# Kernel tuning notes

Hardware: AMD Instinct MI355X
Metric: run time of the kernel (lower is better)

Reference implementation:

```python
import jax, jax.numpy as jnp
import numpy as np

N = 100000      # nodes
E = 1600000     # edges (avg degree 16)
F_IN = 256      # num_features
H2 = 128        # nhid * 2 (layer 1 width)
H = 64          # nhid (layer 2 width)
C = 10          # num_classes


def setup_inputs() -> dict:
    key = jax.random.key(0)
    ks = jax.random.split(key, 8)
    x = jax.random.normal(ks[0], (N, F_IN), dtype=jnp.float32)
    edge_index = jax.random.randint(ks[1], (2, E), 0, N, dtype=jnp.int64)
    W1 = jax.random.normal(ks[2], (F_IN, H2), dtype=jnp.float32) / np.float32(np.sqrt(F_IN))
    b1 = jnp.zeros((H2,), jnp.float32)
    W2 = jax.random.normal(ks[3], (H2, H), dtype=jnp.float32) / np.float32(np.sqrt(H2))
    b2 = jnp.zeros((H,), jnp.float32)
    Wl = jax.random.normal(ks[4], (H, C), dtype=jnp.float32) / np.float32(np.sqrt(H))
    bl = jnp.zeros((C,), jnp.float32)
    return {"x": x, "edge_index": edge_index, "W1": W1, "b1": b1,
            "W2": W2, "b2": b2, "Wl": Wl, "bl": bl}


def reference(x, edge_index, W1, b1, W2, b2, Wl, bl):
    # --- GCN normalization with self-loops (PyG GCNConv default) ---
    loops = jnp.arange(N, dtype=edge_index.dtype)
    src = jnp.concatenate([edge_index[0], loops])  # message sources
    dst = jnp.concatenate([edge_index[1], loops])  # message targets
    deg = jax.ops.segment_sum(jnp.ones(src.shape[0], x.dtype), dst, num_segments=N)
    dinv = jnp.where(deg > 0, jax.lax.rsqrt(deg), 0.0)
    norm = dinv[src] * dinv[dst]                   # [E+N]

    def gcn_conv(h, W, b):
        m = h @ W                                  # transform first (out_channels small)
        agg = jax.ops.segment_sum(m[src] * norm[:, None], dst, num_segments=N)
        return agg + b

    h = jax.nn.relu(gcn_conv(x, W1, b1))           # [N, H2]
    h = jax.nn.relu(gcn_conv(h, W2, b2))           # [N, H]
    logits = h @ Wl + bl                            # [N, C]
    return jax.nn.log_softmax(logits, axis=-1)
```

## Files before the change

kernel.cpp:

```cpp
#include <hip/hip_runtime.h>


typedef unsigned short ushort_t;
typedef unsigned int uint_t;
typedef __attribute__((ext_vector_type(8))) short short8;
typedef __attribute__((ext_vector_type(4))) float floatx4;

static __device__ __forceinline__ ushort_t f2bf(float f) {
    union { float f; uint_t u; } c; c.f = f;
    return (ushort_t)((c.u + 0x8000u) >> 16);
}
static __device__ __forceinline__ float bf2f(ushort_t h) {
    union { uint_t u; float f; } c; c.u = ((uint_t)h) << 16;
    return c.f;
}
static __device__ __forceinline__ float2 up2(uint_t p) {
    union { uint_t u; float f; } lo, hi;
    lo.u = p << 16; hi.u = p & 0xffff0000u;
    return make_float2(lo.f, hi.f);
}
static __device__ __forceinline__ uint_t pk2bf(float a, float b) {
    return ((uint_t)f2bf(b) << 16) | (uint_t)f2bf(a);
}

#define NBMAX 800
#define ECAP  4096

__global__ __launch_bounds__(256) void hist_kernel(
    const int* __restrict__ dst, int* __restrict__ histG, int E, int NB) {
    __shared__ int h[NBMAX];
    for (int i = threadIdx.x; i < NB; i += 256) h[i] = 0;
    __syncthreads();
    int i16 = (blockIdx.x * 256 + threadIdx.x) * 16;
    if (i16 + 15 < E) {
        #pragma unroll
        for (int u = 0; u < 4; u++) {
            int4 d = *(const int4*)(dst + i16 + u * 4);
            atomicAdd(&h[d.x >> 7], 1);
            atomicAdd(&h[d.y >> 7], 1);
            atomicAdd(&h[d.z >> 7], 1);
            atomicAdd(&h[d.w >> 7], 1);
        }
    } else {
        for (int e = i16; e < E; e++) atomicAdd(&h[dst[e] >> 7], 1);
    }
    __syncthreads();
    int* out = histG + (size_t)blockIdx.x * NB;
    for (int i = threadIdx.x; i < NB; i += 256) out[i] = h[i];
}

__global__ __launch_bounds__(256) void scan_bucket(
    int* __restrict__ histG, int* __restrict__ totG, int GB, int NB) {
    int b = blockIdx.x * 256 + threadIdx.x;
    if (b >= NB) return;
    int run = 0;
    int g = 0;
    for (; g + 16 <= GB; g += 16) {
        int vv[16];
        #pragma unroll
        for (int u = 0; u < 16; u++) vv[u] = histG[(size_t)(g + u) * NB + b];
        #pragma unroll
        for (int u = 0; u < 16; u++) {
            histG[(size_t)(g + u) * NB + b] = run;
            run += vv[u];
        }
    }
    for (; g < GB; g++) {
        int v = histG[(size_t)g * NB + b];
        histG[(size_t)g * NB + b] = run;
        run += v;
    }
    totG[b] = run;
}

__global__ void scan_tot(const int* __restrict__ totG, int* __restrict__ bbase,
                         int NB) {
    __shared__ int s[256];
    const int t = threadIdx.x;
    int running = 0;
    int nch = (NB + 255) / 256;
    for (int c = 0; c < nch; c++) {
        int j = c * 256 + t;
        int v = (j < NB) ? totG[j] : 0;
        s[t] = v;
        __syncthreads();
        for (int off = 1; off < 256; off <<= 1) {
            int tmp = (t >= off) ? s[t - off] : 0;
            __syncthreads();
            s[t] += tmp;
            __syncthreads();
        }
        if (j < NB) bbase[j] = s[t] - v + running;
        int ctot = s[255];
        __syncthreads();
        running += ctot;
    }
    if (t == 0) bbase[NB] = running;
}

__global__ __launch_bounds__(256) void scatter_kernel(
    const int* __restrict__ src, const int* __restrict__ dst,
    const int* __restrict__ histG, const int* __restrict__ bbase,
    int* __restrict__ packed, int E, int NB) {
    __shared__ int lbase[NBMAX];
    const int* row = histG + (size_t)blockIdx.x * NB;
    for (int i = threadIdx.x; i < NB; i += 256)
        lbase[i] = bbase[i] + row[i];
    __syncthreads();
    int i16 = (blockIdx.x * 256 + threadIdx.x) * 16;
    if (i16 + 15 < E) {
        #pragma unroll
        for (int u = 0; u < 4; u++) {
            int4 s4 = *(const int4*)(src + i16 + u * 4);
            int4 d4 = *(const int4*)(dst + i16 + u * 4);
            int p;
            p = atomicAdd(&lbase[d4.x >> 7], 1); packed[p] = s4.x | ((d4.x & 127) << 17);
            p = atomicAdd(&lbase[d4.y >> 7], 1); packed[p] = s4.y | ((d4.y & 127) << 17);
            p = atomicAdd(&lbase[d4.z >> 7], 1); packed[p] = s4.z | ((d4.z & 127) << 17);
            p = atomicAdd(&lbase[d4.w >> 7], 1); packed[p] = s4.w | ((d4.w & 127) << 17);
        }
    } else {
        for (int e = i16; e < E; e++) {
            int d = dst[e];
            int p = atomicAdd(&lbase[d >> 7], 1);
            packed[p] = src[e] | ((d & 127) << 17);
        }
    }
}

__global__ __launch_bounds__(256) void bucket_csr(
    const int* __restrict__ packed, const int* __restrict__ bbase,
    int* __restrict__ rowptr, int* __restrict__ csr,
    float* __restrict__ dinv, int N, int NB) {
    __shared__ int ebuf[ECAP];
    __shared__ int cnt[128];
    __shared__ int pl[128];
    __shared__ int s[256];
    const int b = blockIdx.x;
    const int t = threadIdx.x;
    const int lo = bbase[b];
    const int hi = bbase[b + 1];
    int m = hi - lo;
    if (m > ECAP) m = ECAP;
    for (int i = t; i < m; i += 256) ebuf[i] = packed[lo + i];
    if (t < 128) cnt[t] = 0;
    __syncthreads();
    for (int i = t; i < m; i += 256) atomicAdd(&cnt[ebuf[i] >> 17], 1);
    __syncthreads();
    const int node0 = b << 7;
    int c = (t < 128) ? cnt[t] : 0;
    if (t < 128 && node0 + t < N)
        dinv[node0 + t] = rsqrtf((float)(c + 1));
    s[t] = c;
    __syncthreads();
    for (int off = 1; off < 256; off <<= 1) {
        int tmp = (t >= off) ? s[t - off] : 0;
        __syncthreads();
        s[t] += tmp;
        __syncthreads();
    }
    int excl = s[t] - c;
    if (t < 128) {
        pl[t] = excl;
        if (node0 + t <= N) rowptr[node0 + t] = lo + excl;
    }
    __syncthreads();
    for (int i = t; i < m; i += 256) {
        int e = ebuf[i];
        int p = atomicAdd(&pl[e >> 17], 1);
        csr[lo + p] = e & 0x1FFFF;
    }
}

__global__ void wcvt2_kernel(const float* __restrict__ W1, const float* __restrict__ W2,
                             ushort_t* __restrict__ W1t, ushort_t* __restrict__ W2t) {
    int i = blockIdx.x * 256 + threadIdx.x;
    if (i < 256 * 128) {
        int k = i / 128, n = i % 128;
        W1t[n * 256 + k] = f2bf(W1[i]);
    }
    int j = i - 256 * 128;
    if (j >= 0 && j < 128 * 64) {
        int k = j / 64, n = j % 64;
        W2t[n * 128 + k] = f2bf(W2[j]);
    }
}

__global__ __launch_bounds__(256, 4) void gemm1_mfma(
    const float* __restrict__ A, const ushort_t* __restrict__ Bt,
    const float* __restrict__ dinv, ushort_t* __restrict__ out, int M) {
    const int tid = threadIdx.x;
    const int l = tid & 63;
    const int wave = tid >> 6;
    const int lrow = l & 15, hh = l >> 4;
    const int m0 = blockIdx.x * 64 + wave * 16;

    int r0 = m0 + lrow; if (r0 >= M) r0 = M - 1;
    const float* ga = A + (size_t)r0 * 256 + hh * 8;
    const ushort_t* gb = Bt + (size_t)lrow * 256 + hh * 8;

    floatx4 acc[8];
    #pragma unroll
    for (int nt = 0; nt < 8; nt++)
        acc[nt] = (floatx4){0.f, 0.f, 0.f, 0.f};

    #pragma unroll
    for (int kk = 0; kk < 8; kk++) {
        const int k0 = kk * 32;
        float4 u = *(const float4*)(ga + k0);
        float4 v = *(const float4*)(ga + k0 + 4);
        short8 afr;
        afr[0] = (short)f2bf(u.x); afr[1] = (short)f2bf(u.y);
        afr[2] = (short)f2bf(u.z); afr[3] = (short)f2bf(u.w);
        afr[4] = (short)f2bf(v.x); afr[5] = (short)f2bf(v.y);
        afr[6] = (short)f2bf(v.z); afr[7] = (short)f2bf(v.w);
        short8 bfr[8];
        #pragma unroll
        for (int nt = 0; nt < 8; nt++)
            bfr[nt] = *(const short8*)(gb + (size_t)nt * 16 * 256 + k0);
        #pragma unroll
        for (int nt = 0; nt < 8; nt++)
            acc[nt] = __builtin_amdgcn_mfma_f32_16x16x32_bf16(
                afr, bfr[nt], acc[nt], 0, 0, 0);
    }

    const int mbase = m0 + hh * 4;
    float4 dv = *(const float4*)&dinv[mbase];
    float d[4] = {dv.x, dv.y, dv.z, dv.w};
    #pragma unroll
    for (int i = 0; i < 4; i++) {
        int m = mbase + i;
        if (m < M) {
            #pragma unroll
            for (int nt = 0; nt < 8; nt++)
                out[(size_t)m * 128 + nt * 16 + lrow] =
                    f2bf(acc[nt][i] * d[i]);
        }
    }
}

__global__ __launch_bounds__(256, 4) void gemm2_mfma(
    const ushort_t* __restrict__ A, const ushort_t* __restrict__ Bt,
    const float* __restrict__ dinv, ushort_t* __restrict__ out, int M) {
    const int tid = threadIdx.x;
    const int l = tid & 63;
    const int wave = tid >> 6;
    const int lrow = l & 15, hh = l >> 4;
    const int m0 = blockIdx.x * 64 + wave * 16;

    int r0 = m0 + lrow; if (r0 >= M) r0 = M - 1;
    const ushort_t* ga = A + (size_t)r0 * 128 + hh * 8;
    const ushort_t* gb = Bt + (size_t)lrow * 128 + hh * 8;

    floatx4 acc[4];
    #pragma unroll
    for (int nt = 0; nt < 4; nt++)
        acc[nt] = (floatx4){0.f, 0.f, 0.f, 0.f};

    #pragma unroll
    for (int kk = 0; kk < 4; kk++) {
        const int k0 = kk * 32;
        short8 afr = *(const short8*)(ga + k0);
        short8 bfr[4];
        #pragma unroll
        for (int nt = 0; nt < 4; nt++)
            bfr[nt] = *(const short8*)(gb + (size_t)nt * 16 * 128 + k0);
        #pragma unroll
        for (int nt = 0; nt < 4; nt++)
            acc[nt] = __builtin_amdgcn_mfma_f32_16x16x32_bf16(
                afr, bfr[nt], acc[nt], 0, 0, 0);
    }

    const int mbase = m0 + hh * 4;
    float4 dv = *(const float4*)&dinv[mbase];
    float d[4] = {dv.x, dv.y, dv.z, dv.w};
    #pragma unroll
    for (int i = 0; i < 4; i++) {
        int m = mbase + i;
        if (m < M) {
            #pragma unroll
            for (int nt = 0; nt < 4; nt++)
                out[(size_t)m * 64 + nt * 16 + lrow] =
                    f2bf(acc[nt][i] * d[i]);
        }
    }
}

__global__ __launch_bounds__(256) void spmm_relu128(
    const ushort_t* __restrict__ Mm, const int* __restrict__ rowptr,
    const int* __restrict__ csr, const float* __restrict__ dinv,
    const float* __restrict__ bias, ushort_t* __restrict__ out, int n, int doff) {
    int v = (blockIdx.x * 256 + threadIdx.x) >> 6;
    int lane = threadIdx.x & 63;
    if (v >= n) return;
    int jb = rowptr[v];
    int cntn = rowptr[v + 1] - jb;
    const char* Mb = (const char*)Mm;
    const int slot = lane >> 4;
    const int q = lane & 15;
    const uint_t qb = (uint_t)q * 16;

    float2 a0 = {0.f, 0.f}, a1 = a0, a2 = a0, a3 = a0;
    if (slot == 0) {
        uint4 s = *(const uint4*)(Mb + ((size_t)v << 8) + qb);
        a0 = up2(s.x); a1 = up2(s.y); a2 = up2(s.z); a3 = up2(s.w);
    }

    for (int base = 0; base < cntn; base += 64) {
        int m = cntn - base; if (m > 64) m = 64;
        int roff = (base + lane < cntn) ? (csr[jb + base + lane] << 8) : doff;
        int m4 = (m + 3) & ~3;
        int jj = 0;
        for (; jj + 16 <= m4; jj += 16) {
            uint_t o[4];
            #pragma unroll
            for (int t = 0; t < 4; t++)
                o[t] = (uint_t)__shfl(roff, jj + 4 * t + slot) + qb;
            uint4 p[4];
            #pragma unroll
            for (int t = 0; t < 4; t++) p[t] = *(const uint4*)(Mb + o[t]);
            #pragma unroll
            for (int t = 0; t < 4; t++) {
                float2 f;
                f = up2(p[t].x); a0.x += f.x; a0.y += f.y;
                f = up2(p[t].y); a1.x += f.x; a1.y += f.y;
                f = up2(p[t].z); a2.x += f.x; a2.y += f.y;
                f = up2(p[t].w); a3.x += f.x; a3.y += f.y;
            }
        }
        for (; jj < m4; jj += 4) {
            uint_t o = (uint_t)__shfl(roff, jj + slot) + qb;
            uint4 p = *(const uint4*)(Mb + o);
            float2 f;
            f = up2(p.x); a0.x += f.x; a0.y += f.y;
            f = up2(p.y); a1.x += f.x; a1.y += f.y;
            f = up2(p.z); a2.x += f.x; a2.y += f.y;
            f = up2(p.w); a3.x += f.x; a3.y += f.y;
        }
    }
    float r[8] = {a0.x, a0.y, a1.x, a1.y, a2.x, a2.y, a3.x, a3.y};
    #pragma unroll
    for (int i = 0; i < 8; i++) r[i] += __shfl_xor(r[i], 16);
    #pragma unroll
    for (int i = 0; i < 8; i++) r[i] += __shfl_xor(r[i], 32);
    if (slot == 0) {
        float d = dinv[v];
        float4 bv0 = *(const float4*)&bias[q * 8];
        float4 bv1 = *(const float4*)&bias[q * 8 + 4];
        float o0 = fmaxf(d * r[0] + bv0.x, 0.f);
        float o1 = fmaxf(d * r[1] + bv0.y, 0.f);
        float o2 = fmaxf(d * r[2] + bv0.z, 0.f);
        float o3 = fmaxf(d * r[3] + bv0.w, 0.f);
        float o4 = fmaxf(d * r[4] + bv1.x, 0.f);
        float o5 = fmaxf(d * r[5] + bv1.y, 0.f);
        float o6 = fmaxf(d * r[6] + bv1.z, 0.f);
        float o7 = fmaxf(d * r[7] + bv1.w, 0.f);
        uint4 pk;
        pk.x = pk2bf(o0, o1); pk.y = pk2bf(o2, o3);
        pk.z = pk2bf(o4, o5); pk.w = pk2bf(o6, o7);
        *(uint4*)(out + (size_t)v * 128 + q * 8) = pk;
    }
}

__global__ __launch_bounds__(256) void spmm_relu64(
    const ushort_t* __restrict__ Mm, const int* __restrict__ rowptr,
    const int* __restrict__ csr, const float* __restrict__ dinv,
    const float* __restrict__ bias, ushort_t* __restrict__ out, int n, int doff) {
    int v = (blockIdx.x * 256 + threadIdx.x) >> 6;
    int lane = threadIdx.x & 63;
    if (v >= n) return;
    int jb = rowptr[v];
    int cntn = rowptr[v + 1] - jb;
    const char* Mb = (const char*)Mm;
    const int slot = lane >> 3;
    const int q = lane & 7;
    const uint_t qb = (uint_t)q * 16;

    float2 a0 = {0.f, 0.f}, a1 = a0, a2 = a0, a3 = a0;
    if (slot == 0) {
        uint4 s = *(const uint4*)(Mb + ((size_t)v << 7) + qb);
        a0 = up2(s.x); a1 = up2(s.y); a2 = up2(s.z); a3 = up2(s.w);
    }

    for (int base = 0; base < cntn; base += 64) {
        int m = cntn - base; if (m > 64) m = 64;
        int roff = (base + lane < cntn) ? (csr[jb + base + lane] << 7) : doff;
        int m8 = (m + 7) & ~7;
        int jj = 0;
        for (; jj + 16 <= m8; jj += 16) {
            uint_t o[2];
            #pragma unroll
            for (int t = 0; t < 2; t++)
                o[t] = (uint_t)__shfl(roff, jj + 8 * t + slot) + qb;
            uint4 p[2];
            #pragma unroll
            for (int t = 0; t < 2; t++) p[t] = *(const uint4*)(Mb + o[t]);
            #pragma unroll
            for (int t = 0; t < 2; t++) {
                float2 f;
                f = up2(p[t].x); a0.x += f.x; a0.y += f.y;
                f = up2(p[t].y); a1.x += f.x; a1.y += f.y;
                f = up2(p[t].z); a2.x += f.x; a2.y += f.y;
                f = up2(p[t].w); a3.x += f.x; a3.y += f.y;
            }
        }
        for (; jj < m8; jj += 8) {
            uint_t o = (uint_t)__shfl(roff, jj + slot) + qb;
            uint4 p = *(const uint4*)(Mb + o);
            float2 f;
            f = up2(p.x); a0.x += f.x; a0.y += f.y;
            f = up2(p.y); a1.x += f.x; a1.y += f.y;
            f = up2(p.z); a2.x += f.x; a2.y += f.y;
            f = up2(p.w); a3.x += f.x; a3.y += f.y;
        }
    }
    float r[8] = {a0.x, a0.y, a1.x, a1.y, a2.x, a2.y, a3.x, a3.y};
    #pragma unroll
    for (int i = 0; i < 8; i++) r[i] += __shfl_xor(r[i], 8);
    #pragma unroll
    for (int i = 0; i < 8; i++) r[i] += __shfl_xor(r[i], 16);
    #pragma unroll
    for (int i = 0; i < 8; i++) r[i] += __shfl_xor(r[i], 32);
    if (slot == 0) {
        float d = dinv[v];
        float4 bv0 = *(const float4*)&bias[q * 8];
        float4 bv1 = *(const float4*)&bias[q * 8 + 4];
        float o0 = fmaxf(d * r[0] + bv0.x, 0.f);
        float o1 = fmaxf(d * r[1] + bv0.y, 0.f);
        float o2 = fmaxf(d * r[2] + bv0.z, 0.f);
        float o3 = fmaxf(d * r[3] + bv0.w, 0.f);
        float o4 = fmaxf(d * r[4] + bv1.x, 0.f);
        float o5 = fmaxf(d * r[5] + bv1.y, 0.f);
        float o6 = fmaxf(d * r[6] + bv1.z, 0.f);
        float o7 = fmaxf(d * r[7] + bv1.w, 0.f);
        uint4 pk;
        pk.x = pk2bf(o0, o1); pk.y = pk2bf(o2, o3);
        pk.z = pk2bf(o4, o5); pk.w = pk2bf(o6, o7);
        *(uint4*)(out + (size_t)v * 64 + q * 8) = pk;
    }
}

__global__ __launch_bounds__(256) void head_kernel(
    const ushort_t* __restrict__ h2, const float* __restrict__ Wl,
    const float* __restrict__ bl, float* __restrict__ out, int n) {
    __shared__ float Ws[64 * 10];
    __shared__ float bs[10];
    for (int i = threadIdx.x; i < 640; i += 256) Ws[i] = Wl[i];
    if (threadIdx.x < 10) bs[threadIdx.x] = bl[threadIdx.x];
    __syncthreads();
    int v = blockIdx.x * 256 + threadIdx.x;
    if (v >= n) return;
    float acc[10];
    #pragma unroll
    for (int c = 0; c < 10; c++) acc[c] = bs[c];
    const ushort_t* hrow = &h2[(size_t)v * 64];
    #pragma unroll
    for (int k0 = 0; k0 < 64; k0 += 8) {
        short8 hv = *(const short8*)&hrow[k0];
        #pragma unroll
        for (int kk = 0; kk < 8; kk++) {
            float hf = bf2f((ushort_t)hv[kk]);
            #pragma unroll
            for (int c = 0; c < 10; c++)
                acc[c] += hf * Ws[(k0 + kk) * 10 + c];
        }
    }
    float m = acc[0];
    #pragma unroll
    for (int c = 1; c < 10; c++) m = fmaxf(m, acc[c]);
    float s = 0.f;
    #pragma unroll
    for (int c = 0; c < 10; c++) s += expf(acc[c] - m);
    float lse = logf(s);
    #pragma unroll
    for (int c = 0; c < 10; c++) out[(size_t)v * 10 + c] = acc[c] - m - lse;
}

extern "C" void kernel_launch(void* const* d_in, const int* in_sizes, int n_in,
                              void* d_out, int out_size, void* d_ws, size_t ws_size,
                              hipStream_t stream) {
    const float* x   = (const float*)d_in[0];
    const int*   ei  = (const int*)d_in[1];
    const float* W1  = (const float*)d_in[2];
    const float* b1  = (const float*)d_in[3];
    const float* W2  = (const float*)d_in[4];
    const float* b2  = (const float*)d_in[5];
    const float* Wl  = (const float*)d_in[6];
    const float* bl  = (const float*)d_in[7];
    float*       out = (float*)d_out;

    const int N = in_sizes[0] / 256;
    const int E = in_sizes[1] / 2;
    const int* srcI = ei;
    const int* dstI = ei + E;

    const int NB = (N + 127) >> 7;
    const int GB = (E + 4095) / 4096;

    char* ws = (char*)d_ws;
    size_t off = 0;
    auto alloc = [&](size_t bytes) -> void* {
        void* p = ws + off;
        off = (off + bytes + 255) & ~(size_t)255;
        return p;
    };
    int*      histG  = (int*)alloc((size_t)GB * NB * 4);
    int*      totG   = (int*)alloc((size_t)NB * 4);
    int*      bbase  = (int*)alloc((size_t)(NB + 1) * 4);
    int*      packed = (int*)alloc((size_t)E * 4);
    int*      rowptr = (int*)alloc((size_t)(N + 1) * 4);
    float*    dinv   = (float*)alloc((size_t)(N + 128) * 4);
    int*      csr    = (int*)alloc((size_t)E * 4);
    ushort_t* W1t    = (ushort_t*)alloc((size_t)128 * 256 * 2);
    ushort_t* W2t    = (ushort_t*)alloc((size_t)64 * 128 * 2);
    ushort_t* bufA   = (ushort_t*)alloc((size_t)(N + 2) * 128 * 2);
    ushort_t* bufB   = (ushort_t*)alloc((size_t)N * 128 * 2);

    hist_kernel<<<GB, 256, 0, stream>>>(dstI, histG, E, NB);
    scan_bucket<<<(NB + 255) / 256, 256, 0, stream>>>(histG, totG, GB, NB);
    scan_tot<<<1, 256, 0, stream>>>(totG, bbase, NB);
    scatter_kernel<<<GB, 256, 0, stream>>>(srcI, dstI, histG, bbase, packed, E, NB);
    bucket_csr<<<NB, 256, 0, stream>>>(packed, bbase, rowptr, csr, dinv, N, NB);

    wcvt2_kernel<<<(256 * 128 + 128 * 64 + 255) / 256, 256, 0, stream>>>(W1, W2, W1t, W2t);

    const int gblk = (N + 63) / 64;
    gemm1_mfma<<<gblk, 256, 0, stream>>>(x, W1t, dinv, bufA, N);
    hipMemsetAsync(bufA + (size_t)N * 128, 0, 256, stream);
    spmm_relu128<<<(N + 3) / 4, 256, 0, stream>>>(bufA, rowptr, csr, dinv, b1, bufB, N, N << 8);
    gemm2_mfma<<<gblk, 256, 0, stream>>>(bufB, W2t, dinv, bufA, N);
    hipMemsetAsync(bufA + (size_t)N * 64, 0, 128, stream);
    spmm_relu64<<<(N + 3) / 4, 256, 0, stream>>>(bufA, rowptr, csr, dinv, b2, bufB, N, N << 7);
    head_kernel<<<(N + 255) / 256, 256, 0, stream>>>(bufB, Wl, bl, out, N);
}
```

Measured before the change: 395.5 us.

## Stage GEMM A and B tiles in swizzled LDS via direct global-to-LDS loads

Both MFMA GEMM kernels now copy their full A row tile and the whole transposed weight matrix into shared memory using 16-byte global_load_lds, then read MFMA fragments from LDS. An XOR swizzle on the column chunk avoids bank conflicts. This removes repeated per-wave global reads of the weights and lets the loads be issued in bulk. The cost is very large LDS footprints (about 128KB per block in gemm1), which limits occupancy to roughly one block per CU. There is also no overlap between loading and compute, because everything is loaded before a single barrier.

```diff
diff --git a/kernel.cpp b/kernel.cpp
--- a/kernel.cpp
+++ b/kernel.cpp
@@ -21,6 +21,11 @@
 }
 static __device__ __forceinline__ uint_t pk2bf(float a, float b) {
     return ((uint_t)f2bf(b) << 16) | (uint_t)f2bf(a);
+}
+static __device__ __forceinline__ void ld_lds16(void* lds, const void* g) {
+    __builtin_amdgcn_global_load_lds(
+        (const __attribute__((address_space(1))) unsigned int*)g,
+        (__attribute__((address_space(3))) unsigned int*)lds, 16, 0, 0);
 }
 
 #define NBMAX 800
@@ -186,29 +191,45 @@
     }
 }
 
-__global__ __launch_bounds__(256, 4) void gemm1_mfma(
+__global__ __launch_bounds__(256) void gemm1_mfma(
     const float* __restrict__ A, const ushort_t* __restrict__ Bt,
     const float* __restrict__ dinv, ushort_t* __restrict__ out, int M) {
+    __shared__ float    As[64 * 256];
+    __shared__ ushort_t Bs[128 * 256];
     const int tid = threadIdx.x;
     const int l = tid & 63;
     const int wave = tid >> 6;
     const int lrow = l & 15, hh = l >> 4;
-    const int m0 = blockIdx.x * 64 + wave * 16;
-
-    int r0 = m0 + lrow; if (r0 >= M) r0 = M - 1;
-    const float* ga = A + (size_t)r0 * 256 + hh * 8;
-    const ushort_t* gb = Bt + (size_t)lrow * 256 + hh * 8;
+    const int m0 = blockIdx.x * 64;
+
+    #pragma unroll
+    for (int rd = 0; rd < 16; rd++) {
+        int idx = rd * 256 + tid;
+        int r = idx >> 6, cs = idx & 63;
+        int row = m0 + r; if (row >= M) row = M - 1;
+        int cl = cs ^ (r & 7);
+        ld_lds16(&As[idx * 4], A + (size_t)row * 256 + cl * 4);
+    }
+    #pragma unroll
+    for (int rd = 0; rd < 16; rd++) {
+        int idx = rd * 256 + tid;
+        int n = idx >> 5, cs = idx & 31;
+        int cl = cs ^ (n & 7);
+        ld_lds16(&Bs[idx * 8], Bt + (size_t)n * 256 + cl * 8);
+    }
+    __syncthreads();
 
     floatx4 acc[8];
     #pragma unroll
     for (int nt = 0; nt < 8; nt++)
         acc[nt] = (floatx4){0.f, 0.f, 0.f, 0.f};
 
+    const int wr = wave * 16 + lrow;
     #pragma unroll
     for (int kk = 0; kk < 8; kk++) {
-        const int k0 = kk * 32;
-        float4 u = *(const float4*)(ga + k0);
-        float4 v = *(const float4*)(ga + k0 + 4);
+        int c0 = kk * 8 + hh * 2;
+        float4 u = *(const float4*)&As[wr * 256 + ((c0    ) ^ (wr & 7)) * 4];
+        float4 v = *(const float4*)&As[wr * 256 + ((c0 + 1) ^ (wr & 7)) * 4];
         short8 afr;
         afr[0] = (short)f2bf(u.x); afr[1] = (short)f2bf(u.y);
         afr[2] = (short)f2bf(u.z); afr[3] = (short)f2bf(u.w);
@@ -216,15 +237,18 @@
         afr[6] = (short)f2bf(v.z); afr[7] = (short)f2bf(v.w);
         short8 bfr[8];
         #pragma unroll
-        for (int nt = 0; nt < 8; nt++)
-            bfr[nt] = *(const short8*)(gb + (size_t)nt * 16 * 256 + k0);
+        for (int nt = 0; nt < 8; nt++) {
+            int n = nt * 16 + lrow;
+            int c = kk * 4 + hh;
+            bfr[nt] = *(const short8*)&Bs[n * 256 + (c ^ (n & 7)) * 8];
+        }
         #pragma unroll
         for (int nt = 0; nt < 8; nt++)
             acc[nt] = __builtin_amdgcn_mfma_f32_16x16x32_bf16(
                 afr, bfr[nt], acc[nt], 0, 0, 0);
     }
 
-    const int mbase = m0 + hh * 4;
+    const int mbase = m0 + wave * 16 + hh * 4;
     float4 dv = *(const float4*)&dinv[mbase];
     float d[4] = {dv.x, dv.y, dv.z, dv.w};
     #pragma unroll
@@ -239,39 +263,57 @@
     }
 }
 
-__global__ __launch_bounds__(256, 4) void gemm2_mfma(
+__global__ __launch_bounds__(256) void gemm2_mfma(
     const ushort_t* __restrict__ A, const ushort_t* __restrict__ Bt,
     const float* __restrict__ dinv, ushort_t* __restrict__ out, int M) {
+    __shared__ ushort_t As[64 * 128];
+    __shared__ ushort_t Bs[64 * 128];
     const int tid = threadIdx.x;
     const int l = tid & 63;
     const int wave = tid >> 6;
     const int lrow = l & 15, hh = l >> 4;
-    const int m0 = blockIdx.x * 64 + wave * 16;
-
-    int r0 = m0 + lrow; if (r0 >= M) r0 = M - 1;
-    const ushort_t* ga = A + (size_t)r0 * 128 + hh * 8;
-    const ushort_t* gb = Bt + (size_t)lrow * 128 + hh * 8;
+    const int m0 = blockIdx.x * 64;
+
+    #pragma unroll
+    for (int rd = 0; rd < 4; rd++) {
+        int idx = rd * 256 + tid;
+        int r = idx >> 4, cs = idx & 15;
+        int row = m0 + r; if (row >= M) row = M - 1;
+        int cl = cs ^ (r & 7);
+        ld_lds16(&As[idx * 8], A + (size_t)row * 128 + cl * 8);
+    }
+    #pragma unroll
+    for (int rd = 0; rd < 4; rd++) {
+        int idx = rd * 256 + tid;
+        int n = idx >> 4, cs = idx & 15;
+        int cl = cs ^ (n & 7);
+        ld_lds16(&Bs[idx * 8], Bt + (size_t)n * 128 + cl * 8);
+    }
+    __syncthreads();
 
     floatx4 acc[4];
     #pragma unroll
     for (int nt = 0; nt < 4; nt++)
         acc[nt] = (floatx4){0.f, 0.f, 0.f, 0.f};
 
+    const int wr = wave * 16 + lrow;
     #pragma unroll
     for (int kk = 0; kk < 4; kk++) {
-        const int k0 = kk * 32;
-        short8 afr = *(const short8*)(ga + k0);
+        int c0 = kk * 4 + hh;
+        short8 afr = *(const short8*)&As[wr * 128 + (c0 ^ (wr & 7)) * 8];
         short8 bfr[4];
         #pragma unroll
-        for (int nt = 0; nt < 4; nt++)
-            bfr[nt] = *(const short8*)(gb + (size_t)nt * 16 * 128 + k0);
+        for (int nt = 0; nt < 4; nt++) {
+            int n = nt * 16 + lrow;
+            bfr[nt] = *(const short8*)&Bs[n * 128 + (c0 ^ (n & 7)) * 8];
+        }
         #pragma unroll
         for (int nt = 0; nt < 4; nt++)
             acc[nt] = __builtin_amdgcn_mfma_f32_16x16x32_bf16(
                 afr, bfr[nt], acc[nt], 0, 0, 0);
     }
 
-    const int mbase = m0 + hh * 4;
+    const int mbase = m0 + wave * 16 + hh * 4;
     float4 dv = *(const float4*)&dinv[mbase];
     float d[4] = {dv.x, dv.y, dv.z, dv.w};
     #pragma unroll
```

Result: faster. 361.6 us (-8.6%).
